# Performance work log

Measured on AMD Instinct MI355X. Metric: run time of the kernel, lower is better.

The kernel has to match this reference:

```python
import jax, jax.numpy as jnp
import numpy as np

DIM = 512
HEADS = 8
HEAD_DIM = DIM // HEADS
SCALE = HEAD_DIM ** -0.5
EPS = 1e-5


def setup_inputs() -> dict:
    key = jax.random.key(0)
    ks = jax.random.split(key, 6)
    B, N, C = 4, 2048, DIM
    x = jax.random.normal(ks[0], (B, N, C), dtype=jnp.float32)
    w_qkv = jax.random.normal(ks[1], (C, 3 * C), dtype=jnp.float32) * (C ** -0.5)
    w_proj = jax.random.normal(ks[2], (C, C), dtype=jnp.float32) * (C ** -0.5)
    b_proj = jax.random.normal(ks[3], (C,), dtype=jnp.float32) * 0.02
    gamma = jnp.ones((C,), dtype=jnp.float32)
    beta = jnp.zeros((C,), dtype=jnp.float32)
    return {"x": x, "w_qkv": w_qkv, "w_proj": w_proj, "b_proj": b_proj,
            "gamma": gamma, "beta": beta}


def reference(x, w_qkv, w_proj, b_proj, gamma, beta):
    B, N, C = x.shape
    # LayerNorm over channel dim
    mu = jnp.mean(x, axis=-1, keepdims=True)
    var = jnp.mean(jnp.square(x - mu), axis=-1, keepdims=True)
    xn = (x - mu) * jax.lax.rsqrt(var + EPS) * gamma + beta
    # QKV projection (fp32, no bias)
    qkv = xn @ w_qkv  # [B, N, 3C]
    qkv = qkv.reshape(B, N, 3, HEADS, HEAD_DIM)
    q = jnp.transpose(qkv[:, :, 0], (0, 2, 1, 3))  # [B, H, N, D]
    k = jnp.transpose(qkv[:, :, 1], (0, 2, 1, 3))
    v = jnp.transpose(qkv[:, :, 2], (0, 2, 1, 3))
    attn = jnp.einsum('bhnd,bhmd->bhnm', q, k) * SCALE
    attn = jax.nn.softmax(attn, axis=-1)
    out = jnp.einsum('bhnm,bhmd->bhnd', attn, v)  # [B, H, N, D]
    out = jnp.transpose(out, (0, 2, 1, 3)).reshape(B, N, C)
    out = out @ w_proj + b_proj
    return x + out
```

## Files before the change

### kernel.cpp

```cpp
#include <hip/hip_runtime.h>
#include <hip/hip_bf16.h>
#include <math.h>

typedef _Float16 f16;
typedef _Float16 half8 __attribute__((ext_vector_type(8)));
typedef _Float16 half4 __attribute__((ext_vector_type(4)));
typedef float f32x4 __attribute__((ext_vector_type(4)));

#define DIMC 512
#define HEADS 8
#define HD 64
#define BB 4
#define NN 2048
#define MM (BB*NN)
#define NQKV (3*DIMC)
#define SCALE 0.125f
#define LOG2E 1.44269504f
#define EPSLN 1e-5f
#define NCHUNK 4

__device__ __forceinline__ void g2l16(const void* g, void* l) {
    __builtin_amdgcn_global_load_lds(
        (const __attribute__((address_space(1))) unsigned int*)g,
        (__attribute__((address_space(3))) unsigned int*)l, 16, 0, 0);
}

__global__ __launch_bounds__(256) void ln_kernel(const float* __restrict__ x,
                                                 const float* __restrict__ gamma,
                                                 const float* __restrict__ beta,
                                                 f16* __restrict__ xn) {
    int w = threadIdx.x >> 6;
    int lane = threadIdx.x & 63;
    int row = blockIdx.x * 4 + w;
    const float* xr = x + (size_t)row * DIMC;
    float4 v0 = ((const float4*)xr)[lane * 2];
    float4 v1 = ((const float4*)xr)[lane * 2 + 1];
    float s = v0.x + v0.y + v0.z + v0.w + v1.x + v1.y + v1.z + v1.w;
#pragma unroll
    for (int off = 1; off < 64; off <<= 1) s += __shfl_xor(s, off);
    float mu = s * (1.0f / DIMC);
    float d0 = v0.x - mu, d1 = v0.y - mu, d2 = v0.z - mu, d3 = v0.w - mu;
    float d4 = v1.x - mu, d5 = v1.y - mu, d6 = v1.z - mu, d7 = v1.w - mu;
    float s2 = d0*d0 + d1*d1 + d2*d2 + d3*d3 + d4*d4 + d5*d5 + d6*d6 + d7*d7;
#pragma unroll
    for (int off = 1; off < 64; off <<= 1) s2 += __shfl_xor(s2, off);
    float rstd = rsqrtf(s2 * (1.0f / DIMC) + EPSLN);
    float4 g0 = ((const float4*)gamma)[lane * 2];
    float4 g1 = ((const float4*)gamma)[lane * 2 + 1];
    float4 b0 = ((const float4*)beta)[lane * 2];
    float4 b1 = ((const float4*)beta)[lane * 2 + 1];
    half8 o;
    o[0] = (f16)(d0 * rstd * g0.x + b0.x);
    o[1] = (f16)(d1 * rstd * g0.y + b0.y);
    o[2] = (f16)(d2 * rstd * g0.z + b0.z);
    o[3] = (f16)(d3 * rstd * g0.w + b0.w);
    o[4] = (f16)(d4 * rstd * g1.x + b1.x);
    o[5] = (f16)(d5 * rstd * g1.y + b1.y);
    o[6] = (f16)(d6 * rstd * g1.z + b1.z);
    o[7] = (f16)(d7 * rstd * g1.w + b1.w);
    ((half8*)(xn + (size_t)row * DIMC))[lane] = o;
}

__global__ __launch_bounds__(256) void transpose_cast(const float* __restrict__ src,
                                                      f16* __restrict__ dst,
                                                      int R, int C) {
    __shared__ f16 t[32][72];
    int k0 = blockIdx.y * 32, n0 = blockIdx.x * 64;
    int tid = threadIdx.x;
    int rr = tid >> 6, col = tid & 63;
#pragma unroll
    for (int p = 0; p < 8; p++) {
        int r = p * 4 + rr;
        t[r][col] = (f16)src[(size_t)(k0 + r) * C + n0 + col];
    }
    __syncthreads();
    int nl = tid >> 2, kc = (tid & 3) * 8;
    half8 v;
#pragma unroll
    for (int j = 0; j < 8; j++) v[j] = t[kc + j][nl];
    *(half8*)&dst[(size_t)(n0 + nl) * R + k0 + kc] = v;
}

__device__ __forceinline__ void gemm128_loop(const char* Ag, const char* Bg,
                                             f16* As, f16* Bs, f32x4 (&acc)[4][4]) {
    int tid = threadIdx.x;
    int w = tid >> 6, lane = tid & 63, l15 = lane & 15, quad = lane >> 4;
    int wy = w >> 1, wx = w & 1;
    int off0 = w * 1024 + lane * 16;
    for (int kk = 0; kk < 16; ++kk) {
        __syncthreads();
#pragma unroll
        for (int c = 0; c < 2; ++c) {
            int off = c * 4096 + off0;
            int row = off >> 6, col = off & 63;
            g2l16(Ag + (size_t)row * 1024 + kk * 64 + col, (char*)As + c * 4096 + w * 1024);
            g2l16(Bg + (size_t)row * 1024 + kk * 64 + col, (char*)Bs + c * 4096 + w * 1024);
        }
        __syncthreads();
        half8 af[4], bf[4];
#pragma unroll
        for (int i = 0; i < 4; ++i) {
            af[i] = *(const half8*)((const char*)As + ((wy * 64 + i * 16 + l15) << 6) + quad * 16);
            bf[i] = *(const half8*)((const char*)Bs + ((wx * 64 + i * 16 + l15) << 6) + quad * 16);
        }
#pragma unroll
        for (int i = 0; i < 4; ++i)
#pragma unroll
            for (int j = 0; j < 4; ++j)
                acc[i][j] = __builtin_amdgcn_mfma_f32_16x16x32_f16(af[i], bf[j], acc[i][j], 0, 0, 0);
    }
}

__global__ __launch_bounds__(256) void gemm_qkv(const f16* __restrict__ xn,
                                                const f16* __restrict__ wt,
                                                f16* __restrict__ qb,
                                                f16* __restrict__ kbuf,
                                                f16* __restrict__ vtb) {
    __shared__ __align__(16) f16 As[128 * 32];
    __shared__ __align__(16) f16 Bs[128 * 32];
    int tid = threadIdx.x;
    int w = tid >> 6, lane = tid & 63, l15 = lane & 15, quad = lane >> 4;
    int wy = w >> 1, wx = w & 1;
    int m0 = blockIdx.y * 128, c0 = blockIdx.x * 128;
    f32x4 acc[4][4] = {};
    gemm128_loop((const char*)(xn + (size_t)m0 * DIMC),
                 (const char*)(wt + (size_t)c0 * DIMC), As, Bs, acc);
    int bx = blockIdx.x;
    if (bx < 8) {
        const float QS = SCALE * LOG2E;
        f16* dst = (bx < 4) ? qb : kbuf;
        float mul = (bx < 4) ? QS : 1.0f;
        int cb = (bx < 4) ? c0 : c0 - DIMC;
#pragma unroll
        for (int i = 0; i < 4; ++i)
#pragma unroll
            for (int j = 0; j < 4; ++j)
#pragma unroll
                for (int r = 0; r < 4; ++r) {
                    int m = m0 + wy * 64 + i * 16 + quad * 4 + r;
                    int c = cb + wx * 64 + j * 16 + l15;
                    int b = m >> 11, n = m & 2047;
                    int h = c >> 6, d = c & 63;
                    dst[(((size_t)(b * HEADS + h)) * NN + n) * HD + d] = (f16)(acc[i][j][r] * mul);
                }
    } else {
        __syncthreads();
        f16* T = (f16*)As + w * 512;
        int cb = c0 - 2 * DIMC;
        int dl = lane >> 2, mp = lane & 3;
#pragma unroll
        for (int i = 0; i < 4; ++i)
#pragma unroll
            for (int j = 0; j < 4; ++j) {
                half4 hv;
#pragma unroll
                for (int r = 0; r < 4; ++r) hv[r] = (f16)acc[i][j][r];
                *(half4*)&T[l15 * 20 + quad * 4] = hv;
                half4 rv = *(half4*)&T[dl * 20 + mp * 4];
                int c = cb + wx * 64 + j * 16 + dl;
                int m = m0 + wy * 64 + i * 16 + mp * 4;
                int b = m >> 11, n = m & 2047;
                int h = c >> 6, d = c & 63;
                *(half4*)&vtb[(((size_t)(b * HEADS + h)) * HD + d) * NN + n] = rv;
            }
    }
}

__global__ __launch_bounds__(256, 4) void attn_kernel(const f16* __restrict__ qb,
                                                      const f16* __restrict__ kbuf,
                                                      const f16* __restrict__ vtb,
                                                      f16* __restrict__ po,
                                                      float2* __restrict__ pml) {
    __shared__ __align__(16) f16 Ks[64 * 72];
    __shared__ __align__(16) f16 Vs[64 * 72];
    int bh = blockIdx.y;
    int chunk = blockIdx.z;
    int n0 = blockIdx.x * 128;
    int tid = threadIdx.x, w = tid >> 6, lane = tid & 63, l15 = lane & 15, quad = lane >> 4;
    const f16* Kbase = kbuf + (size_t)bh * NN * HD;
    const f16* Vbase = vtb + (size_t)bh * HD * NN;
    const f16* Qbase = qb + (size_t)bh * NN * HD;
    half8 qf[2][2];
#pragma unroll
    for (int qt = 0; qt < 2; ++qt) {
        const f16* qr = Qbase + (size_t)(n0 + w * 32 + qt * 16 + l15) * HD + quad * 8;
        qf[qt][0] = *(const half8*)qr;
        qf[qt][1] = *(const half8*)(qr + 32);
    }
    f32x4 ot[2][4] = {};
    float m_run[2] = {-INFINITY, -INFINITY};
    float l_run[2] = {0.f, 0.f};
    int srow = tid >> 2, part = (tid & 3) * 16;
    int kbeg = chunk * (NN / NCHUNK);
    half8 kp0, kp1, vp0, vp1;
    {
        const f16* kg = Kbase + (size_t)(kbeg + srow) * HD + part;
        kp0 = ((const half8*)kg)[0]; kp1 = ((const half8*)kg)[1];
        const f16* vg = Vbase + (size_t)srow * NN + kbeg + part;
        vp0 = ((const half8*)vg)[0]; vp1 = ((const half8*)vg)[1];
    }
    for (int it = 0; it < NN / NCHUNK / 64; ++it) {
        __syncthreads();
        *(half8*)&Ks[srow * 72 + part] = kp0;
        *(half8*)&Ks[srow * 72 + part + 8] = kp1;
        *(half8*)&Vs[srow * 72 + part] = vp0;
        *(half8*)&Vs[srow * 72 + part + 8] = vp1;
        __syncthreads();
        if (it < NN / NCHUNK / 64 - 1) {
            int kt0 = kbeg + (it + 1) * 64;
            const f16* kg = Kbase + (size_t)(kt0 + srow) * HD + part;
            kp0 = ((const half8*)kg)[0]; kp1 = ((const half8*)kg)[1];
            const f16* vg = Vbase + (size_t)srow * NN + kt0 + part;
            vp0 = ((const half8*)vg)[0]; vp1 = ((const half8*)vg)[1];
        }
        f32x4 s0[4], s1[4];
#pragma unroll
        for (int kt = 0; kt < 4; ++kt) {
            half8 a0 = *(const half8*)&Ks[(kt * 16 + l15) * 72 + quad * 8];
            half8 a1 = *(const half8*)&Ks[(kt * 16 + l15) * 72 + 32 + quad * 8];
            f32x4 z0 = {};
            z0 = __builtin_amdgcn_mfma_f32_16x16x32_f16(a0, qf[0][0], z0, 0, 0, 0);
            z0 = __builtin_amdgcn_mfma_f32_16x16x32_f16(a1, qf[0][1], z0, 0, 0, 0);
            s0[kt] = z0;
            f32x4 z1 = {};
            z1 = __builtin_amdgcn_mfma_f32_16x16x32_f16(a0, qf[1][0], z1, 0, 0, 0);
            z1 = __builtin_amdgcn_mfma_f32_16x16x32_f16(a1, qf[1][1], z1, 0, 0, 0);
            s1[kt] = z1;
        }
        half4 pb[2][4];
#pragma unroll
        for (int qt = 0; qt < 2; ++qt) {
            f32x4* s = (qt == 0) ? s0 : s1;
            float tmax = -INFINITY;
#pragma unroll
            for (int kt = 0; kt < 4; ++kt)
#pragma unroll
                for (int r = 0; r < 4; ++r) tmax = fmaxf(tmax, s[kt][r]);
            tmax = fmaxf(tmax, __shfl_xor(tmax, 16));
            tmax = fmaxf(tmax, __shfl_xor(tmax, 32));
            float m_new = fmaxf(m_run[qt], tmax);
            float alpha = __builtin_amdgcn_exp2f(m_run[qt] - m_new);
            m_run[qt] = m_new;
            float lsum = 0.f;
#pragma unroll
            for (int kt = 0; kt < 4; ++kt)
#pragma unroll
                for (int r = 0; r < 4; ++r) {
                    float p = __builtin_amdgcn_exp2f(s[kt][r] - m_new);
                    s[kt][r] = p;
                    lsum += p;
                }
            lsum += __shfl_xor(lsum, 16);
            lsum += __shfl_xor(lsum, 32);
            l_run[qt] = l_run[qt] * alpha + lsum;
#pragma unroll
            for (int dt = 0; dt < 4; ++dt)
#pragma unroll
                for (int r = 0; r < 4; ++r) ot[qt][dt][r] *= alpha;
#pragma unroll
            for (int kt = 0; kt < 4; ++kt) {
                half4 pk;
#pragma unroll
                for (int r = 0; r < 4; ++r) pk[r] = (f16)s[kt][r];
                pb[qt][kt] = pk;
            }
        }
#pragma unroll
        for (int kt = 0; kt < 4; ++kt)
#pragma unroll
            for (int dt = 0; dt < 4; ++dt) {
                half4 av = *(const half4*)&Vs[(dt * 16 + l15) * 72 + kt * 16 + quad * 4];
                ot[0][dt] = __builtin_amdgcn_mfma_f32_16x16x16f16(av, pb[0][kt], ot[0][dt], 0, 0, 0);
                ot[1][dt] = __builtin_amdgcn_mfma_f32_16x16x16f16(av, pb[1][kt], ot[1][dt], 0, 0, 0);
            }
    }
    size_t rowbase = ((size_t)chunk * (BB * HEADS) + bh) * NN;
#pragma unroll
    for (int qt = 0; qt < 2; ++qt) {
        int n = n0 + w * 32 + qt * 16 + l15;
        if (quad == 0) {
            float2 ml; ml.x = m_run[qt]; ml.y = l_run[qt];
            pml[rowbase + n] = ml;
        }
#pragma unroll
        for (int dt = 0; dt < 4; ++dt) {
            half4 hv;
#pragma unroll
            for (int r = 0; r < 4; ++r) hv[r] = (f16)ot[qt][dt][r];
            *(half4*)&po[(rowbase + n) * HD + dt * 16 + quad * 4] = hv;
        }
    }
}

__global__ __launch_bounds__(256) void attn_combine(const f16* __restrict__ po,
                                                    const float2* __restrict__ pml,
                                                    f16* __restrict__ ao) {
    int gid = blockIdx.x * 256 + threadIdx.x;
    int row = gid >> 3, d0 = (gid & 7) * 8;
    int bh = row >> 11, n = row & 2047;
    const int CS = BB * HEADS * NN;
    float2 ml[NCHUNK];
    float M = -INFINITY;
#pragma unroll
    for (int c = 0; c < NCHUNK; ++c) {
        ml[c] = pml[row + c * CS];
        M = fmaxf(M, ml[c].x);
    }
    float a[NCHUNK], denom = 0.f;
#pragma unroll
    for (int c = 0; c < NCHUNK; ++c) {
        a[c] = __builtin_amdgcn_exp2f(ml[c].x - M);
        denom += ml[c].y * a[c];
    }
    float inv = 1.0f / denom;
    float acc[8] = {};
#pragma unroll
    for (int c = 0; c < NCHUNK; ++c) {
        half8 oc = *(const half8*)&po[((size_t)row + c * CS) * HD + d0];
#pragma unroll
        for (int j = 0; j < 8; ++j) acc[j] += (float)oc[j] * a[c];
    }
    half8 r;
#pragma unroll
    for (int j = 0; j < 8; ++j) r[j] = (f16)(acc[j] * inv);
    int h = bh & 7, b = bh >> 3;
    *(half8*)&ao[((size_t)(b * NN + n)) * DIMC + h * HD + d0] = r;
}

__global__ __launch_bounds__(256) void gemm_proj(const f16* __restrict__ aob,
                                                 const f16* __restrict__ wt,
                                                 const float* __restrict__ x,
                                                 const float* __restrict__ bias,
                                                 float* __restrict__ out) {
    __shared__ __align__(16) f16 As[128 * 32];
    __shared__ __align__(16) f16 Bs[64 * 32];
    int tid = threadIdx.x;
    int w = tid >> 6, lane = tid & 63, l15 = lane & 15, quad = lane >> 4;
    int m0 = blockIdx.y * 128, c0 = blockIdx.x * 64;
    const char* Ag = (const char*)(aob + (size_t)m0 * DIMC);
    const char* Bg = (const char*)(wt + (size_t)c0 * DIMC);
    f32x4 acc[2][4] = {};
    int off0 = w * 1024 + lane * 16;
    for (int kk = 0; kk < 16; ++kk) {
        __syncthreads();
#pragma unroll
        for (int c = 0; c < 2; ++c) {
            int off = c * 4096 + off0;
            int row = off >> 6, col = off & 63;
            g2l16(Ag + (size_t)row * 1024 + kk * 64 + col, (char*)As + c * 4096 + w * 1024);
        }
        {
            int off = tid * 16;
            int row = off >> 6, col = off & 63;
            g2l16(Bg + (size_t)row * 1024 + kk * 64 + col, (char*)Bs + w * 1024);
        }
        __syncthreads();
        half8 af[2], bf[4];
#pragma unroll
        for (int i = 0; i < 2; ++i)
            af[i] = *(const half8*)((const char*)As + ((w * 32 + i * 16 + l15) << 6) + quad * 16);
#pragma unroll
        for (int j = 0; j < 4; ++j)
            bf[j] = *(const half8*)((const char*)Bs + ((j * 16 + l15) << 6) + quad * 16);
#pragma unroll
        for (int i = 0; i < 2; ++i)
#pragma unroll
            for (int j = 0; j < 4; ++j)
                acc[i][j] = __builtin_amdgcn_mfma_f32_16x16x32_f16(af[i], bf[j], acc[i][j], 0, 0, 0);
    }
#pragma unroll
    for (int i = 0; i < 2; ++i)
#pragma unroll
        for (int j = 0; j < 4; ++j)
#pragma unroll
            for (int r = 0; r < 4; ++r) {
                int m = m0 + w * 32 + i * 16 + quad * 4 + r;
                int c = c0 + j * 16 + l15;
                out[(size_t)m * DIMC + c] = x[(size_t)m * DIMC + c] + bias[c] + acc[i][j][r];
            }
}

extern "C" void kernel_launch(void* const* d_in, const int* in_sizes, int n_in,
                              void* d_out, int out_size, void* d_ws, size_t ws_size,
                              hipStream_t stream) {
    (void)in_sizes; (void)n_in; (void)out_size; (void)ws_size;
    const float* x     = (const float*)d_in[0];
    const float* wqkv  = (const float*)d_in[1];
    const float* wproj = (const float*)d_in[2];
    const float* bproj = (const float*)d_in[3];
    const float* gamma = (const float*)d_in[4];
    const float* beta  = (const float*)d_in[5];
    float* out = (float*)d_out;

    char* ws = (char*)d_ws;
    f16* xn     = (f16*)ws;                 ws += (size_t)MM * DIMC * 2;
    f16* wqkvt  = (f16*)ws;                 ws += (size_t)NQKV * DIMC * 2;
    f16* wprojt = (f16*)ws;                 ws += (size_t)DIMC * DIMC * 2;
    f16* qbuf   = (f16*)ws;                 ws += (size_t)MM * DIMC * 2;
    f16* kbuf   = (f16*)ws;                 ws += (size_t)MM * DIMC * 2;
    f16* vtbuf  = (f16*)ws;                 ws += (size_t)MM * DIMC * 2;
    f16* aobuf  = (f16*)ws;                 ws += (size_t)MM * DIMC * 2;
    f16* po     = (f16*)ws;                 ws += (size_t)NCHUNK * BB * HEADS * NN * HD * 2;
    float2* pml = (float2*)ws;              ws += (size_t)NCHUNK * BB * HEADS * NN * sizeof(float2);

    ln_kernel<<<MM / 4, 256, 0, stream>>>(x, gamma, beta, xn);
    transpose_cast<<<dim3(NQKV / 64, DIMC / 32), 256, 0, stream>>>(wqkv, wqkvt, DIMC, NQKV);
    transpose_cast<<<dim3(DIMC / 64, DIMC / 32), 256, 0, stream>>>(wproj, wprojt, DIMC, DIMC);
    gemm_qkv<<<dim3(NQKV / 128, MM / 128), 256, 0, stream>>>(xn, wqkvt, qbuf, kbuf, vtbuf);
    attn_kernel<<<dim3(NN / 128, BB * HEADS, NCHUNK), 256, 0, stream>>>(qbuf, kbuf, vtbuf, po, pml);
    attn_combine<<<(BB * HEADS * NN * HD / 8) / 256, 256, 0, stream>>>(po, pml, aobuf);
    gemm_proj<<<dim3(DIMC / 64, MM / 128), 256, 0, stream>>>(aobuf, wprojt, x, bproj, out);
}
```

Measured before the change: 184.8 us.

## Merge prep kernels and use lazy rescale with MFMA row sums in attention

LayerNorm and both weight transpose-casts are merged into a single prep launch, saving two kernel launches. In attention, the online-softmax rescale of the output accumulators is skipped when no lane's running max increases. The per-row exp sum is now computed by an MFMA against a ones vector instead of scalar adds and shuffles. The row sum now accumulates from fp16-rounded probabilities, which slightly changes numerics, and the extra MFMAs add matrix-core work.

```diff
diff --git a/kernel.cpp b/kernel.cpp
--- a/kernel.cpp
+++ b/kernel.cpp
@@ -25,13 +25,13 @@
         (__attribute__((address_space(3))) unsigned int*)l, 16, 0, 0);
 }
 
-__global__ __launch_bounds__(256) void ln_kernel(const float* __restrict__ x,
-                                                 const float* __restrict__ gamma,
-                                                 const float* __restrict__ beta,
-                                                 f16* __restrict__ xn) {
+__device__ __forceinline__ void ln_rows(const float* __restrict__ x,
+                                        const float* __restrict__ gamma,
+                                        const float* __restrict__ beta,
+                                        f16* __restrict__ xn, int blk) {
     int w = threadIdx.x >> 6;
     int lane = threadIdx.x & 63;
-    int row = blockIdx.x * 4 + w;
+    int row = blk * 4 + w;
     const float* xr = x + (size_t)row * DIMC;
     float4 v0 = ((const float4*)xr)[lane * 2];
     float4 v1 = ((const float4*)xr)[lane * 2 + 1];
@@ -61,11 +61,10 @@
     ((half8*)(xn + (size_t)row * DIMC))[lane] = o;
 }
 
-__global__ __launch_bounds__(256) void transpose_cast(const float* __restrict__ src,
-                                                      f16* __restrict__ dst,
-                                                      int R, int C) {
+__device__ __forceinline__ void transp_tile(const float* __restrict__ src,
+                                            f16* __restrict__ dst,
+                                            int R, int C, int k0, int n0) {
     __shared__ f16 t[32][72];
-    int k0 = blockIdx.y * 32, n0 = blockIdx.x * 64;
     int tid = threadIdx.x;
     int rr = tid >> 6, col = tid & 63;
 #pragma unroll
@@ -79,6 +78,28 @@
 #pragma unroll
     for (int j = 0; j < 8; j++) v[j] = t[kc + j][nl];
     *(half8*)&dst[(size_t)(n0 + nl) * R + k0 + kc] = v;
+}
+
+__global__ __launch_bounds__(256) void prep_kernel(const float* __restrict__ x,
+                                                   const float* __restrict__ gamma,
+                                                   const float* __restrict__ beta,
+                                                   const float* __restrict__ wqkv,
+                                                   const float* __restrict__ wproj,
+                                                   f16* __restrict__ xn,
+                                                   f16* __restrict__ wqkvt,
+                                                   f16* __restrict__ wprojt) {
+    int bid = blockIdx.x;
+    if (bid < 2048) {
+        ln_rows(x, gamma, beta, xn, bid);
+    } else if (bid < 2048 + 384) {
+        int b2 = bid - 2048;
+        int bx = b2 % 24, by = b2 / 24;
+        transp_tile(wqkv, wqkvt, DIMC, NQKV, by * 32, bx * 64);
+    } else {
+        int b2 = bid - 2048 - 384;
+        int bx = b2 % 8, by = b2 / 8;
+        transp_tile(wproj, wprojt, DIMC, DIMC, by * 32, bx * 64);
+    }
 }
 
 __device__ __forceinline__ void gemm128_loop(const char* Ag, const char* Bg,
@@ -188,8 +209,11 @@
         qf[qt][1] = *(const half8*)(qr + 32);
     }
     f32x4 ot[2][4] = {};
+    f32x4 lacc[2] = {};
     float m_run[2] = {-INFINITY, -INFINITY};
-    float l_run[2] = {0.f, 0.f};
+    half4 ones;
+#pragma unroll
+    for (int j = 0; j < 4; ++j) ones[j] = (f16)1.0f;
     int srow = tid >> 2, part = (tid & 3) * 16;
     int kbeg = chunk * (NN / NCHUNK);
     half8 kp0, kp1, vp0, vp1;
@@ -238,48 +262,45 @@
                 for (int r = 0; r < 4; ++r) tmax = fmaxf(tmax, s[kt][r]);
             tmax = fmaxf(tmax, __shfl_xor(tmax, 16));
             tmax = fmaxf(tmax, __shfl_xor(tmax, 32));
-            float m_new = fmaxf(m_run[qt], tmax);
-            float alpha = __builtin_amdgcn_exp2f(m_run[qt] - m_new);
-            m_run[qt] = m_new;
-            float lsum = 0.f;
-#pragma unroll
-            for (int kt = 0; kt < 4; ++kt)
-#pragma unroll
-                for (int r = 0; r < 4; ++r) {
-                    float p = __builtin_amdgcn_exp2f(s[kt][r] - m_new);
-                    s[kt][r] = p;
-                    lsum += p;
-                }
-            lsum += __shfl_xor(lsum, 16);
-            lsum += __shfl_xor(lsum, 32);
-            l_run[qt] = l_run[qt] * alpha + lsum;
-#pragma unroll
-            for (int dt = 0; dt < 4; ++dt)
-#pragma unroll
-                for (int r = 0; r < 4; ++r) ot[qt][dt][r] *= alpha;
+            if (__any(tmax > m_run[qt])) {
+                float m_new = fmaxf(m_run[qt], tmax);
+                float alpha = __builtin_amdgcn_exp2f(m_run[qt] - m_new);
+                m_run[qt] = m_new;
+#pragma unroll
+                for (int dt = 0; dt < 4; ++dt)
+#pragma unroll
+                    for (int r = 0; r < 4; ++r) ot[qt][dt][r] *= alpha;
+#pragma unroll
+                for (int r = 0; r < 4; ++r) lacc[qt][r] *= alpha;
+            }
+            float mq = m_run[qt];
 #pragma unroll
             for (int kt = 0; kt < 4; ++kt) {
                 half4 pk;
 #pragma unroll
-                for (int r = 0; r < 4; ++r) pk[r] = (f16)s[kt][r];
+                for (int r = 0; r < 4; ++r)
+                    pk[r] = (f16)__builtin_amdgcn_exp2f(s[kt][r] - mq);
                 pb[qt][kt] = pk;
             }
         }
 #pragma unroll
-        for (int kt = 0; kt < 4; ++kt)
+        for (int kt = 0; kt < 4; ++kt) {
+            lacc[0] = __builtin_amdgcn_mfma_f32_16x16x16f16(ones, pb[0][kt], lacc[0], 0, 0, 0);
+            lacc[1] = __builtin_amdgcn_mfma_f32_16x16x16f16(ones, pb[1][kt], lacc[1], 0, 0, 0);
 #pragma unroll
             for (int dt = 0; dt < 4; ++dt) {
                 half4 av = *(const half4*)&Vs[(dt * 16 + l15) * 72 + kt * 16 + quad * 4];
                 ot[0][dt] = __builtin_amdgcn_mfma_f32_16x16x16f16(av, pb[0][kt], ot[0][dt], 0, 0, 0);
                 ot[1][dt] = __builtin_amdgcn_mfma_f32_16x16x16f16(av, pb[1][kt], ot[1][dt], 0, 0, 0);
             }
+        }
     }
     size_t rowbase = ((size_t)chunk * (BB * HEADS) + bh) * NN;
 #pragma unroll
     for (int qt = 0; qt < 2; ++qt) {
         int n = n0 + w * 32 + qt * 16 + l15;
         if (quad == 0) {
-            float2 ml; ml.x = m_run[qt]; ml.y = l_run[qt];
+            float2 ml; ml.x = m_run[qt]; ml.y = lacc[qt][0];
             pml[rowbase + n] = ml;
         }
 #pragma unroll
@@ -403,9 +424,8 @@
     f16* po     = (f16*)ws;                 ws += (size_t)NCHUNK * BB * HEADS * NN * HD * 2;
     float2* pml = (float2*)ws;              ws += (size_t)NCHUNK * BB * HEADS * NN * sizeof(float2);
 
-    ln_kernel<<<MM / 4, 256, 0, stream>>>(x, gamma, beta, xn);
-    transpose_cast<<<dim3(NQKV / 64, DIMC / 32), 256, 0, stream>>>(wqkv, wqkvt, DIMC, NQKV);
-    transpose_cast<<<dim3(DIMC / 64, DIMC / 32), 256, 0, stream>>>(wproj, wprojt, DIMC, DIMC);
+    prep_kernel<<<2048 + 384 + 128, 256, 0, stream>>>(x, gamma, beta, wqkv, wproj,
+                                                      xn, wqkvt, wprojt);
     gemm_qkv<<<dim3(NQKV / 128, MM / 128), 256, 0, stream>>>(xn, wqkvt, qbuf, kbuf, vtbuf);
     attn_kernel<<<dim3(NN / 128, BB * HEADS, NCHUNK), 256, 0, stream>>>(qbuf, kbuf, vtbuf, po, pml);
     attn_combine<<<(BB * HEADS * NN * HD / 8) / 256, 256, 0, stream>>>(po, pml, aobuf);
```

Result: no change. 188.2 us (+1.9%).
